# Kernel optimization log

Hardware: AMD Instinct MI355X
Metric: run time of the kernel (lower is better)

The kernel has to match this reference:

```python
import jax, jax.numpy as jnp
import numpy as np

T = 2048          # num tokens (single long prefill sequence)
HID = 2048        # hidden_size
NH = 16           # num query heads
NKV = 2           # num kv heads
HD = 128          # head_dim (kv_channels)
ROPE_BASE = 10000.0


def setup_inputs() -> dict:
    key = jax.random.key(0)
    k1, k2, k3, k4, k5 = jax.random.split(key, 5)
    s = 0.02
    return {
        "hidden_states": jax.random.normal(k1, (T, HID), dtype=jnp.float32),
        "positions": jnp.arange(T, dtype=jnp.int64 if jax.config.jax_enable_x64 else jnp.int32),
        "Wq": jax.random.normal(k2, (NH * HD, HID), dtype=jnp.float32) * s,
        "Wk": jax.random.normal(k3, (NKV * HD, HID), dtype=jnp.float32) * s,
        "Wv": jax.random.normal(k4, (NKV * HD, HID), dtype=jnp.float32) * s,
        "Wo": jax.random.normal(k5, (HID, NH * HD), dtype=jnp.float32) * s,
    }


def _rope_cos_sin(positions):
    # fp32 RoPE tables, HF-style (concat of freqs with itself)
    inv_freq = 1.0 / (ROPE_BASE ** (jnp.arange(0, HD, 2, dtype=jnp.float32) / HD))
    freqs = positions.astype(jnp.float32)[:, None] * inv_freq[None, :]   # [T, HD/2]
    emb = jnp.concatenate([freqs, freqs], axis=-1)                        # [T, HD]
    return jnp.cos(emb)[:, None, :], jnp.sin(emb)[:, None, :]             # [T,1,HD]


def _rotate_half(x):
    x1, x2 = jnp.split(x, 2, axis=-1)
    return jnp.concatenate([-x2, x1], axis=-1)


def reference(hidden_states, positions, Wq, Wk, Wv, Wo):
    dtype = hidden_states.dtype
    # fused QKV projection (weights concatenated once, single GEMM)
    W_fused = jnp.concatenate([Wq, Wk, Wv], axis=0)            # [q+2kv, HID]
    qkv = hidden_states @ W_fused.T                             # [T, q+2kv]
    q, k, v = jnp.split(qkv, [NH * HD, NH * HD + NKV * HD], axis=-1)

    # fp32 RoPE on q/k
    cos, sin = _rope_cos_sin(positions)                         # [T,1,HD]
    qf = q.reshape(T, NH, HD).astype(jnp.float32)
    kf = k.reshape(T, NKV, HD).astype(jnp.float32)
    qf = qf * cos + _rotate_half(qf) * sin
    kf = kf * cos + _rotate_half(kf) * sin
    q = qf.astype(dtype)                                        # [T,NH,HD]
    k = kf.astype(dtype)                                        # [T,NKV,HD]
    v = v.reshape(T, NKV, HD)

    # causal GQA attention (same math as the paged-attention kernel on one seq)
    group = NH // NKV
    k_rep = jnp.repeat(k, group, axis=1)                        # [T,NH,HD]
    v_rep = jnp.repeat(v, group, axis=1)                        # [T,NH,HD]
    scale = HD ** -0.5
    scores = jnp.einsum('qhd,khd->hqk', q, k_rep) * scale       # [NH,T,T]
    causal = jnp.tril(jnp.ones((T, T), dtype=bool))
    scores = jnp.where(causal[None], scores, jnp.finfo(scores.dtype).min)
    probs = jax.nn.softmax(scores, axis=-1)
    attn = jnp.einsum('hqk,khd->qhd', probs, v_rep).reshape(T, NH * HD)

    return attn @ Wo.T                                          # [T, HID]
```

## Files before the change

### kernel.cpp

```cpp
#include <hip/hip_runtime.h>

#define T_TOK 2048
#define HID   2048
#define NH    16
#define NKV   2
#define HD    128
#define QDIM  (NH * HD)
#define KVDIM (NKV * HD)
#define QKVDIM (QDIM + 2 * KVDIM)

typedef float          f32x4  __attribute__((ext_vector_type(4)));
typedef unsigned short u16x8  __attribute__((ext_vector_type(8)));
typedef __bf16         bf16x8 __attribute__((ext_vector_type(8)));

__device__ __forceinline__ unsigned short f2bf(float f) {
    unsigned int u = __builtin_bit_cast(unsigned int, f);
    u += 0x7fffu + ((u >> 16) & 1u);
    return (unsigned short)(u >> 16);
}

__device__ __forceinline__ f32x4 mfma16(u16x8 a, u16x8 b, f32x4 c) {
    return __builtin_amdgcn_mfma_f32_16x16x32_bf16(
        __builtin_bit_cast(bf16x8, a), __builtin_bit_cast(bf16x8, b), c, 0, 0, 0);
}

__global__ __launch_bounds__(256) void pack_bf16_all(
    const float* __restrict__ hidden, const float* __restrict__ Wq,
    const float* __restrict__ Wk, const float* __restrict__ Wv,
    const float* __restrict__ Wo,
    unsigned short* __restrict__ hb, unsigned short* __restrict__ Wf,
    unsigned short* __restrict__ Wob)
{
    const int b = blockIdx.x;
    const float* src; unsigned short* dst; size_t off;
    if      (b < 2048) { src = hidden; dst = hb;            off = (size_t)b * 2048; }
    else if (b < 4096) { src = Wq;     dst = Wf;            off = (size_t)(b - 2048) * 2048; }
    else if (b < 4352) { src = Wk;     dst = Wf + 4194304;  off = (size_t)(b - 4096) * 2048; }
    else if (b < 4608) { src = Wv;     dst = Wf + 4718592;  off = (size_t)(b - 4352) * 2048; }
    else               { src = Wo;     dst = Wob;           off = (size_t)(b - 4608) * 2048; }

    const size_t i = off + threadIdx.x * 8;
    float4 f0 = *reinterpret_cast<const float4*>(src + i);
    float4 f1 = *reinterpret_cast<const float4*>(src + i + 4);
    u16x8 o;
    o[0]=f2bf(f0.x); o[1]=f2bf(f0.y); o[2]=f2bf(f0.z); o[3]=f2bf(f0.w);
    o[4]=f2bf(f1.x); o[5]=f2bf(f1.y); o[6]=f2bf(f1.z); o[7]=f2bf(f1.w);
    *reinterpret_cast<u16x8*>(dst + i) = o;
}

__global__ __launch_bounds__(256) void gemm_bf16(
    const unsigned short* __restrict__ A,
    const unsigned short* __restrict__ B,
    float* __restrict__ C,
    int K, int NC)
{
    __shared__ alignas(16) unsigned short As[2][128 * 64];
    __shared__ alignas(16) unsigned short Bs[2][128 * 64];

    const int tid  = threadIdx.x;
    const int lane = tid & 63;
    const int w    = tid >> 6;
    const int lg   = lane >> 4, lc = lane & 15;
    const int m0   = blockIdx.y * 128, n0 = blockIdx.x * 128;

    const int rowL = lane >> 3;
    const int gS   = (lane & 7) ^ rowL;
    const int wr   = (w >> 1) * 64, wc = (w & 1) * 64;

    f32x4 acc[4][4] = {};

    auto stage = [&](int buf, int kb) {
        #pragma unroll
        for (int ci = 0; ci < 4; ci++) {
            const int chunk = w * 4 + ci;
            const int row   = chunk * 8 + rowL;
            const unsigned short* gpA = &A[(size_t)(m0 + row) * K + kb + gS * 8];
            __builtin_amdgcn_global_load_lds(
                (const __attribute__((address_space(1))) void*)gpA,
                (__attribute__((address_space(3))) void*)(&As[buf][chunk * 512]),
                16, 0, 0);
            const unsigned short* gpB = &B[(size_t)(n0 + row) * K + kb + gS * 8];
            __builtin_amdgcn_global_load_lds(
                (const __attribute__((address_space(1))) void*)gpB,
                (__attribute__((address_space(3))) void*)(&Bs[buf][chunk * 512]),
                16, 0, 0);
        }
    };

    stage(0, 0);
    const int nk = K >> 6;
    for (int t = 0; t < nk; ++t) {
        asm volatile("s_waitcnt vmcnt(0)" ::: "memory");
        __syncthreads();
        if (t + 1 < nk) stage((t + 1) & 1, (t + 1) * 64);

        const unsigned short* As_ = As[t & 1];
        const unsigned short* Bs_ = Bs[t & 1];
        #pragma unroll
        for (int kk = 0; kk < 2; kk++) {
            u16x8 af[4], bf[4];
            #pragma unroll
            for (int mi = 0; mi < 4; mi++) {
                const int r = wr + mi * 16 + lc;
                const int g = (kk * 4 + lg) ^ (lc & 7);
                af[mi] = *reinterpret_cast<const u16x8*>(&As_[r * 64 + g * 8]);
            }
            #pragma unroll
            for (int ni = 0; ni < 4; ni++) {
                const int r = wc + ni * 16 + lc;
                const int g = (kk * 4 + lg) ^ (lc & 7);
                bf[ni] = *reinterpret_cast<const u16x8*>(&Bs_[r * 64 + g * 8]);
            }
            #pragma unroll
            for (int mi = 0; mi < 4; mi++)
                #pragma unroll
                for (int ni = 0; ni < 4; ni++)
                    acc[mi][ni] = mfma16(af[mi], bf[ni], acc[mi][ni]);
        }
        __syncthreads();
    }

    #pragma unroll
    for (int mi = 0; mi < 4; mi++)
        #pragma unroll
        for (int ni = 0; ni < 4; ni++)
            #pragma unroll
            for (int j = 0; j < 4; j++)
                C[(size_t)(m0 + wr + mi * 16 + lg * 4 + j) * NC
                  + n0 + wc + ni * 16 + lc] = acc[mi][ni][j];
}

__global__ __launch_bounds__(256) void rope_kernel(
    const float* __restrict__ qkv,
    const int* __restrict__ positions,
    unsigned short* __restrict__ qr,
    unsigned short* __restrict__ kr)
{
    const int t   = blockIdx.x;
    const int tid = threadIdx.x;
    __shared__ float cosv[64], sinv[64];

    if (tid < 64) {
        float invf = expf(-(float)tid * 0.14391156831212787f);
        float f = (float)positions[t] * invf;
        cosv[tid] = cosf(f);
        sinv[tid] = sinf(f);
    }
    __syncthreads();

    const float* row = qkv + (size_t)t * QKVDIM;

    for (int i = tid; i < NH * 64; i += 256) {
        int hh = i >> 6, j = i & 63;
        float x1 = row[hh * HD + j];
        float x2 = row[hh * HD + j + 64];
        float c = cosv[j], s = sinv[j];
        qr[(size_t)t * QDIM + hh * HD + j]      = f2bf(x1 * c - x2 * s);
        qr[(size_t)t * QDIM + hh * HD + j + 64] = f2bf(x2 * c + x1 * s);
    }
    if (tid < NKV * 64) {
        int hh = tid >> 6, j = tid & 63;
        float x1 = row[QDIM + hh * HD + j];
        float x2 = row[QDIM + hh * HD + j + 64];
        float c = cosv[j], s = sinv[j];
        kr[(size_t)t * KVDIM + hh * HD + j]      = f2bf(x1 * c - x2 * s);
        kr[(size_t)t * KVDIM + hh * HD + j + 64] = f2bf(x2 * c + x1 * s);
    }
}

__global__ __launch_bounds__(256) void v_transpose(
    const float* __restrict__ qkv,
    unsigned short* __restrict__ vt)
{
    __shared__ unsigned short tile[64][72];
    const int tid = threadIdx.x;
    const int t0  = blockIdx.x * 64;
    const int d0  = blockIdx.y * 64;

    {
        int r = tid >> 2;
        int c = (tid & 3) * 16;
        const float* src = &qkv[(size_t)(t0 + r) * QKVDIM + QDIM + KVDIM + d0 + c];
        #pragma unroll
        for (int i = 0; i < 4; i++) {
            float4 f = *reinterpret_cast<const float4*>(src + i * 4);
            tile[r][c + i*4 + 0] = f2bf(f.x);
            tile[r][c + i*4 + 1] = f2bf(f.y);
            tile[r][c + i*4 + 2] = f2bf(f.z);
            tile[r][c + i*4 + 3] = f2bf(f.w);
        }
    }
    __syncthreads();
    {
        int dr = tid >> 3;
        int tc = (tid & 7) * 8;
        #pragma unroll
        for (int i = 0; i < 2; i++) {
            int d = dr + i * 32;
            u16x8 ov;
            #pragma unroll
            for (int e = 0; e < 8; e++) ov[e] = tile[tc + e][d];
            *reinterpret_cast<u16x8*>(&vt[(size_t)(d0 + d) * T_TOK + t0 + tc]) = ov;
        }
    }
}

__global__ __launch_bounds__(256) void attn_kernel(
    const unsigned short* __restrict__ q,
    const unsigned short* __restrict__ k,
    const unsigned short* __restrict__ vt,
    unsigned short* __restrict__ o,
    float* __restrict__ pO,
    float* __restrict__ pML)
{
    __shared__ alignas(16) unsigned short Ks[2][64 * 128];
    __shared__ alignas(16) unsigned short Vs[2][128 * 64];
    __shared__ alignas(16) unsigned short P[4][16][72];

    const int tid  = threadIdx.x;
    const int lane = tid & 63;
    const int w    = tid >> 6;
    const int lg   = lane >> 4, lc = lane & 15;
    const int b    = blockIdx.x;
    const int h    = b & 15;
    const int idx  = b >> 4;

    int tau, c0;
    if (idx <= 16)      { tau = 15 + idx; c0 = 0; }
    else if (idx == 17) { tau = 31;       c0 = 1; }
    else {
        int j = idx - 18, kk = 15 - (j >> 1);
        if ((j & 1) == 0) { tau = kk - 1;  c0 = 0; }
        else              { tau = kk + 15; c0 = 1; }
    }
    const int kstart = c0 << 4;
    const int kcnt   = min(16, tau + 1 - kstart);

    const int q0   = tau * 64 + w * 16;
    const int hk   = h >> 3;
    const float scale = 0.08838834764831845f;
    const int xr   = (lc & 7) << 4;

    const int krow_l = (lane >> 4);
    const int kgS    = (lane & 15);
    const int vrow_l = (lane >> 3);
    const int vgS    = (lane & 7);

    u16x8 qf[4];
    #pragma unroll
    for (int dc = 0; dc < 4; dc++)
        qf[dc] = *reinterpret_cast<const u16x8*>(
            &q[(size_t)(q0 + lc) * QDIM + h * HD + dc * 32 + lg * 8]);

    float mrow = -1e30f, ell = 0.f;
    f32x4 oacc[8] = {};

    auto stage = [&](int buf, int kb) {
        #pragma unroll
        for (int ci = 0; ci < 4; ci++) {
            const int chunk = w * 4 + ci;
            const int row   = chunk * 4 + krow_l;
            const int gSk   = kgS ^ (row & 7);
            const unsigned short* gp =
                &k[(size_t)(kb + row) * KVDIM + hk * HD + gSk * 8];
            __builtin_amdgcn_global_load_lds(
                (const __attribute__((address_space(1))) void*)gp,
                (__attribute__((address_space(3))) void*)(&Ks[buf][chunk * 512]),
                16, 0, 0);
        }
        #pragma unroll
        for (int ci = 0; ci < 4; ci++) {
            const int chunk = w * 4 + ci;
            const int dr    = chunk * 8 + vrow_l;
            const int gSv   = vgS ^ (dr & 7);
            const unsigned short* gp =
                &vt[(size_t)(hk * HD + dr) * T_TOK + kb + gSv * 8];
            __builtin_amdgcn_global_load_lds(
                (const __attribute__((address_space(1))) void*)gp,
                (__attribute__((address_space(3))) void*)(&Vs[buf][chunk * 512]),
                16, 0, 0);
        }
    };

    stage(0, kstart * 64);
    for (int it = 0; it < kcnt; ++it) {
        asm volatile("s_waitcnt vmcnt(0)" ::: "memory");
        __syncthreads();
        if (it + 1 < kcnt) stage((it + 1) & 1, (kstart + it + 1) * 64);

        const int kb = (kstart + it) * 64;
        const char* KsB = (const char*)Ks[it & 1];
        const char* VsB = (const char*)Vs[it & 1];

        float sc[4][4];
        #pragma unroll
        for (int c4 = 0; c4 < 4; c4++) {
            const int row = c4 * 16 + lc;
            f32x4 s = {0.f, 0.f, 0.f, 0.f};
            #pragma unroll
            for (int dc = 0; dc < 4; dc++) {
                u16x8 kf = *reinterpret_cast<const u16x8*>(
                    KsB + row * 256 + ((dc * 64 + lg * 16) ^ xr));
                s = mfma16(kf, qf[dc], s);
            }
            #pragma unroll
            for (int j = 0; j < 4; j++) {
                const int kpos = kb + c4 * 16 + lg * 4 + j;
                const int qrow = q0 + lc;
                sc[c4][j] = (kpos <= qrow) ? s[j] * scale : -1e30f;
            }
        }

        float t01 = fmaxf(fmaxf(sc[0][0], sc[0][1]), fmaxf(sc[0][2], sc[0][3]));
        float t23 = fmaxf(fmaxf(sc[1][0], sc[1][1]), fmaxf(sc[1][2], sc[1][3]));
        float t45 = fmaxf(fmaxf(sc[2][0], sc[2][1]), fmaxf(sc[2][2], sc[2][3]));
        float t67 = fmaxf(fmaxf(sc[3][0], sc[3][1]), fmaxf(sc[3][2], sc[3][3]));
        float tmx = fmaxf(fmaxf(t01, t23), fmaxf(t45, t67));
        tmx = fmaxf(tmx, __shfl_xor(tmx, 16));
        tmx = fmaxf(tmx, __shfl_xor(tmx, 32));

        float mn;
        if (__all(tmx <= mrow + 8.0f)) {
            mn = mrow;
        } else {
            mn = fmaxf(mrow, tmx);
            float alpha = __expf(mrow - mn);
            mrow = mn;
            ell *= alpha;
            float aj[4];
            #pragma unroll
            for (int j = 0; j < 4; j++)
                aj[j] = __shfl(alpha, lg * 4 + j);
            #pragma unroll
            for (int d8 = 0; d8 < 8; d8++)
                #pragma unroll
                for (int j = 0; j < 4; j++)
                    oacc[d8][j] *= aj[j];
        }

        float rs = 0.f;
        #pragma unroll
        for (int c4 = 0; c4 < 4; c4++) {
            float p0 = __expf(sc[c4][0] - mn);
            float p1 = __expf(sc[c4][1] - mn);
            float p2 = __expf(sc[c4][2] - mn);
            float p3 = __expf(sc[c4][3] - mn);
            rs += (p0 + p1) + (p2 + p3);
            ushort4 pk;
            pk.x = f2bf(p0); pk.y = f2bf(p1); pk.z = f2bf(p2); pk.w = f2bf(p3);
            *reinterpret_cast<ushort4*>(&P[w][lc][c4 * 16 + lg * 4]) = pk;
        }
        rs += __shfl_xor(rs, 16);
        rs += __shfl_xor(rs, 32);
        ell += rs;

        asm volatile("s_waitcnt lgkmcnt(0)" ::: "memory");
        __builtin_amdgcn_sched_barrier(0);

        u16x8 pf0 = *reinterpret_cast<const u16x8*>(&P[w][lc][lg * 8]);
        u16x8 pf1 = *reinterpret_cast<const u16x8*>(&P[w][lc][32 + lg * 8]);

        #pragma unroll
        for (int d8 = 0; d8 < 8; d8++) {
            const int drow = d8 * 16 + lc;
            u16x8 vf0 = *reinterpret_cast<const u16x8*>(
                VsB + drow * 128 + ((lg * 16) ^ xr));
            u16x8 vf1 = *reinterpret_cast<const u16x8*>(
                VsB + drow * 128 + ((lg * 16 + 64) ^ xr));
            oacc[d8] = mfma16(pf0, vf0, oacc[d8]);
            oacc[d8] = mfma16(pf1, vf1, oacc[d8]);
        }
        __syncthreads();
    }

    if (tau < 16) {
        float ej[4];
        #pragma unroll
        for (int j = 0; j < 4; j++)
            ej[j] = __shfl(ell, lg * 4 + j);
        #pragma unroll
        for (int d8 = 0; d8 < 8; d8++)
            #pragma unroll
            for (int j = 0; j < 4; j++) {
                float val = oacc[d8][j] / ej[j];
                o[(size_t)(q0 + lg * 4 + j) * QDIM + h * HD + d8 * 16 + lc] = f2bf(val);
            }
    } else {
        const int s = (h * 16 + (tau - 16)) * 2 + c0;
        float* po = pO + (size_t)s * 8192;
        #pragma unroll
        for (int d8 = 0; d8 < 8; d8++)
            #pragma unroll
            for (int j = 0; j < 4; j++)
                po[(w * 16 + lg * 4 + j) * 128 + d8 * 16 + lc] = oacc[d8][j];
        if (lg == 0) {
            pML[s * 128 + w * 16 + lc]      = mrow;
            pML[s * 128 + 64 + w * 16 + lc] = ell;
        }
    }
}

__global__ __launch_bounds__(256) void attn_combine(
    const float* __restrict__ pO,
    const float* __restrict__ pML,
    unsigned short* __restrict__ o)
{
    const int b  = blockIdx.x;
    const int h  = b >> 4, ti = b & 15;
    const int tau = 16 + ti;
    const int s0 = (h * 16 + ti) * 2, s1 = s0 + 1;

    const int tid = threadIdx.x;
    const int r   = tid >> 2;
    const int cg  = (tid & 3) * 32;

    const float m1 = pML[s0 * 128 + r],      m2 = pML[s1 * 128 + r];
    const float l1 = pML[s0 * 128 + 64 + r], l2 = pML[s1 * 128 + 64 + r];
    const float M  = fmaxf(m1, m2);
    const float w1 = __expf(m1 - M), w2 = __expf(m2 - M);
    const float rn = 1.0f / (w1 * l1 + w2 * l2);

    const float* o1 = pO + (size_t)s0 * 8192 + r * 128 + cg;
    const float* o2 = pO + (size_t)s1 * 8192 + r * 128 + cg;
    unsigned short* dst = o + (size_t)(tau * 64 + r) * QDIM + h * HD + cg;

    #pragma unroll
    for (int i = 0; i < 8; i++) {
        float4 a = *reinterpret_cast<const float4*>(o1 + i * 4);
        float4 c = *reinterpret_cast<const float4*>(o2 + i * 4);
        ushort4 pk;
        pk.x = f2bf((w1 * a.x + w2 * c.x) * rn);
        pk.y = f2bf((w1 * a.y + w2 * c.y) * rn);
        pk.z = f2bf((w1 * a.z + w2 * c.z) * rn);
        pk.w = f2bf((w1 * a.w + w2 * c.w) * rn);
        *reinterpret_cast<ushort4*>(dst + i * 4) = pk;
    }
}

extern "C" void kernel_launch(void* const* d_in, const int* in_sizes, int n_in,
                              void* d_out, int out_size, void* d_ws, size_t ws_size,
                              hipStream_t stream) {
    const float* hidden    = (const float*)d_in[0];
    const int*   positions = (const int*)d_in[1];
    const float* Wq        = (const float*)d_in[2];
    const float* Wk        = (const float*)d_in[3];
    const float* Wv        = (const float*)d_in[4];
    const float* Wo        = (const float*)d_in[5];
    float*       out       = (float*)d_out;

    char* ws = (char*)d_ws;
    float*          qkv = (float*)(ws);
    unsigned short* qr  = (unsigned short*)(ws + 20971520);
    unsigned short* kr  = (unsigned short*)(ws + 29360128);
    unsigned short* vt  = (unsigned short*)(ws + 30408704);
    unsigned short* att = (unsigned short*)(ws + 31457280);
    unsigned short* hb  = (unsigned short*)(ws + 39845888);
    unsigned short* Wf  = (unsigned short*)(ws + 48234496);
    unsigned short* Wob = (unsigned short*)(ws + 58720256);
    float* pO  = (float*)(ws);
    float* pML = (float*)(ws + 16777216);

    pack_bf16_all<<<6656, 256, 0, stream>>>(hidden, Wq, Wk, Wv, Wo, hb, Wf, Wob);
    gemm_bf16<<<dim3(QKVDIM / 128, T_TOK / 128), 256, 0, stream>>>(hb, Wf, qkv, HID, QKVDIM);
    rope_kernel<<<T_TOK, 256, 0, stream>>>(qkv, positions, qr, kr);
    v_transpose<<<dim3(T_TOK / 64, KVDIM / 64), 256, 0, stream>>>(qkv, vt);
    attn_kernel<<<NH * 48, 256, 0, stream>>>(qr, kr, vt, att, pO, pML);
    attn_combine<<<256, 256, 0, stream>>>(pO, pML, att);
    gemm_bf16<<<dim3(HID / 128, T_TOK / 128), 256, 0, stream>>>(att, Wob, out, QDIM, HID);
}
```

Baseline: 147.8 us.

## Emit bf16 QKV, prefetch before wait, fold softmax scale into Q, use exp2

The QKV GEMM now writes bf16 instead of fp32, which halves that intermediate traffic and lets rope and the V transpose read bf16. In both GEMMs and attention, the next tile's load is issued before waiting on only the older loads, so the copy overlaps compute. The GEMM also remaps block indices in an XCD-aware pattern across the 8 dies. The softmax scale times log2(e) is folded into Q during rope, so attention uses raw exp2 and masks only diagonal tiles. The lazy-rescale threshold is widened to match the base-2 scale, and storing QKV in bf16 adds a rounding step before rope.

```diff
diff --git a/kernel.cpp b/kernel.cpp
--- a/kernel.cpp
+++ b/kernel.cpp
@@ -14,15 +14,20 @@
 typedef __bf16         bf16x8 __attribute__((ext_vector_type(8)));
 
 __device__ __forceinline__ unsigned short f2bf(float f) {
-    unsigned int u = __builtin_bit_cast(unsigned int, f);
-    u += 0x7fffu + ((u >> 16) & 1u);
-    return (unsigned short)(u >> 16);
+    __bf16 h = (__bf16)f;
+    return __builtin_bit_cast(unsigned short, h);
+}
+__device__ __forceinline__ float bf2f(unsigned short u) {
+    return (float)__builtin_bit_cast(__bf16, u);
 }
 
 __device__ __forceinline__ f32x4 mfma16(u16x8 a, u16x8 b, f32x4 c) {
     return __builtin_amdgcn_mfma_f32_16x16x32_bf16(
         __builtin_bit_cast(bf16x8, a), __builtin_bit_cast(bf16x8, b), c, 0, 0, 0);
 }
+
+#define QSCL 0.12751743f
+#define DEFER_THR 11.5416f
 
 __global__ __launch_bounds__(256) void pack_bf16_all(
     const float* __restrict__ hidden, const float* __restrict__ Wq,
@@ -48,11 +53,12 @@
     *reinterpret_cast<u16x8*>(dst + i) = o;
 }
 
+template<bool BF16OUT>
 __global__ __launch_bounds__(256) void gemm_bf16(
     const unsigned short* __restrict__ A,
     const unsigned short* __restrict__ B,
-    float* __restrict__ C,
-    int K, int NC)
+    void* __restrict__ Cv,
+    int K, int NC, int nbx)
 {
     __shared__ alignas(16) unsigned short As[2][128 * 64];
     __shared__ alignas(16) unsigned short Bs[2][128 * 64];
@@ -61,7 +67,10 @@
     const int lane = tid & 63;
     const int w    = tid >> 6;
     const int lg   = lane >> 4, lc = lane & 15;
-    const int m0   = blockIdx.y * 128, n0 = blockIdx.x * 128;
+
+    const int cpx = gridDim.x >> 3;
+    const int wg  = (blockIdx.x & 7) * cpx + (blockIdx.x >> 3);
+    const int m0  = (wg / nbx) * 128, n0 = (wg % nbx) * 128;
 
     const int rowL = lane >> 3;
     const int gS   = (lane & 7) ^ rowL;
@@ -90,9 +99,13 @@
     stage(0, 0);
     const int nk = K >> 6;
     for (int t = 0; t < nk; ++t) {
-        asm volatile("s_waitcnt vmcnt(0)" ::: "memory");
+        if (t + 1 < nk) {
+            stage((t + 1) & 1, (t + 1) * 64);
+            asm volatile("s_waitcnt vmcnt(8)" ::: "memory");
+        } else {
+            asm volatile("s_waitcnt vmcnt(0)" ::: "memory");
+        }
         __syncthreads();
-        if (t + 1 < nk) stage((t + 1) & 1, (t + 1) * 64);
 
         const unsigned short* As_ = As[t & 1];
         const unsigned short* Bs_ = Bs[t & 1];
@@ -125,13 +138,18 @@
         #pragma unroll
         for (int ni = 0; ni < 4; ni++)
             #pragma unroll
-            for (int j = 0; j < 4; j++)
-                C[(size_t)(m0 + wr + mi * 16 + lg * 4 + j) * NC
-                  + n0 + wc + ni * 16 + lc] = acc[mi][ni][j];
+            for (int j = 0; j < 4; j++) {
+                const size_t idx = (size_t)(m0 + wr + mi * 16 + lg * 4 + j) * NC
+                                   + n0 + wc + ni * 16 + lc;
+                if constexpr (BF16OUT)
+                    ((unsigned short*)Cv)[idx] = f2bf(acc[mi][ni][j]);
+                else
+                    ((float*)Cv)[idx] = acc[mi][ni][j];
+            }
 }
 
 __global__ __launch_bounds__(256) void rope_kernel(
-    const float* __restrict__ qkv,
+    const unsigned short* __restrict__ qkvb,
     const int* __restrict__ positions,
     unsigned short* __restrict__ qr,
     unsigned short* __restrict__ kr)
@@ -148,20 +166,20 @@
     }
     __syncthreads();
 
-    const float* row = qkv + (size_t)t * QKVDIM;
+    const unsigned short* row = qkvb + (size_t)t * QKVDIM;
 
     for (int i = tid; i < NH * 64; i += 256) {
         int hh = i >> 6, j = i & 63;
-        float x1 = row[hh * HD + j];
-        float x2 = row[hh * HD + j + 64];
+        float x1 = bf2f(row[hh * HD + j]);
+        float x2 = bf2f(row[hh * HD + j + 64]);
         float c = cosv[j], s = sinv[j];
-        qr[(size_t)t * QDIM + hh * HD + j]      = f2bf(x1 * c - x2 * s);
-        qr[(size_t)t * QDIM + hh * HD + j + 64] = f2bf(x2 * c + x1 * s);
+        qr[(size_t)t * QDIM + hh * HD + j]      = f2bf((x1 * c - x2 * s) * QSCL);
+        qr[(size_t)t * QDIM + hh * HD + j + 64] = f2bf((x2 * c + x1 * s) * QSCL);
     }
     if (tid < NKV * 64) {
         int hh = tid >> 6, j = tid & 63;
-        float x1 = row[QDIM + hh * HD + j];
-        float x2 = row[QDIM + hh * HD + j + 64];
+        float x1 = bf2f(row[QDIM + hh * HD + j]);
+        float x2 = bf2f(row[QDIM + hh * HD + j + 64]);
         float c = cosv[j], s = sinv[j];
         kr[(size_t)t * KVDIM + hh * HD + j]      = f2bf(x1 * c - x2 * s);
         kr[(size_t)t * KVDIM + hh * HD + j + 64] = f2bf(x2 * c + x1 * s);
@@ -169,7 +187,7 @@
 }
 
 __global__ __launch_bounds__(256) void v_transpose(
-    const float* __restrict__ qkv,
+    const unsigned short* __restrict__ qkvb,
     unsigned short* __restrict__ vt)
 {
     __shared__ unsigned short tile[64][72];
@@ -180,15 +198,10 @@
     {
         int r = tid >> 2;
         int c = (tid & 3) * 16;
-        const float* src = &qkv[(size_t)(t0 + r) * QKVDIM + QDIM + KVDIM + d0 + c];
-        #pragma unroll
-        for (int i = 0; i < 4; i++) {
-            float4 f = *reinterpret_cast<const float4*>(src + i * 4);
-            tile[r][c + i*4 + 0] = f2bf(f.x);
-            tile[r][c + i*4 + 1] = f2bf(f.y);
-            tile[r][c + i*4 + 2] = f2bf(f.z);
-            tile[r][c + i*4 + 3] = f2bf(f.w);
-        }
+        const unsigned short* src =
+            &qkvb[(size_t)(t0 + r) * QKVDIM + QDIM + KVDIM + d0 + c];
+        *reinterpret_cast<u16x8*>(&tile[r][c])     = *reinterpret_cast<const u16x8*>(src);
+        *reinterpret_cast<u16x8*>(&tile[r][c + 8]) = *reinterpret_cast<const u16x8*>(src + 8);
     }
     __syncthreads();
     {
@@ -238,7 +251,6 @@
 
     const int q0   = tau * 64 + w * 16;
     const int hk   = h >> 3;
-    const float scale = 0.08838834764831845f;
     const int xr   = (lc & 7) << 4;
 
     const int krow_l = (lane >> 4);
@@ -284,15 +296,20 @@
 
     stage(0, kstart * 64);
     for (int it = 0; it < kcnt; ++it) {
-        asm volatile("s_waitcnt vmcnt(0)" ::: "memory");
+        if (it + 1 < kcnt) {
+            stage((it + 1) & 1, (kstart + it + 1) * 64);
+            asm volatile("s_waitcnt vmcnt(8)" ::: "memory");
+        } else {
+            asm volatile("s_waitcnt vmcnt(0)" ::: "memory");
+        }
         __syncthreads();
-        if (it + 1 < kcnt) stage((it + 1) & 1, (kstart + it + 1) * 64);
 
         const int kb = (kstart + it) * 64;
         const char* KsB = (const char*)Ks[it & 1];
         const char* VsB = (const char*)Vs[it & 1];
 
         float sc[4][4];
+        const bool dia = (kb + 63 > q0);
         #pragma unroll
         for (int c4 = 0; c4 < 4; c4++) {
             const int row = c4 * 16 + lc;
@@ -303,11 +320,15 @@
                     KsB + row * 256 + ((dc * 64 + lg * 16) ^ xr));
                 s = mfma16(kf, qf[dc], s);
             }
-            #pragma unroll
-            for (int j = 0; j < 4; j++) {
-                const int kpos = kb + c4 * 16 + lg * 4 + j;
-                const int qrow = q0 + lc;
-                sc[c4][j] = (kpos <= qrow) ? s[j] * scale : -1e30f;
+            if (dia) {
+                #pragma unroll
+                for (int j = 0; j < 4; j++) {
+                    const int kpos = kb + c4 * 16 + lg * 4 + j;
+                    sc[c4][j] = (kpos <= q0 + lc) ? s[j] : -1e30f;
+                }
+            } else {
+                #pragma unroll
+                for (int j = 0; j < 4; j++) sc[c4][j] = s[j];
             }
         }
 
@@ -320,11 +341,11 @@
         tmx = fmaxf(tmx, __shfl_xor(tmx, 32));
 
         float mn;
-        if (__all(tmx <= mrow + 8.0f)) {
+        if (__all(tmx <= mrow + DEFER_THR)) {
             mn = mrow;
         } else {
             mn = fmaxf(mrow, tmx);
-            float alpha = __expf(mrow - mn);
+            float alpha = __builtin_amdgcn_exp2f(mrow - mn);
             mrow = mn;
             ell *= alpha;
             float aj[4];
@@ -341,10 +362,10 @@
         float rs = 0.f;
         #pragma unroll
         for (int c4 = 0; c4 < 4; c4++) {
-            float p0 = __expf(sc[c4][0] - mn);
-            float p1 = __expf(sc[c4][1] - mn);
-            float p2 = __expf(sc[c4][2] - mn);
-            float p3 = __expf(sc[c4][3] - mn);
+            float p0 = __builtin_amdgcn_exp2f(sc[c4][0] - mn);
+            float p1 = __builtin_amdgcn_exp2f(sc[c4][1] - mn);
+            float p2 = __builtin_amdgcn_exp2f(sc[c4][2] - mn);
+            float p3 = __builtin_amdgcn_exp2f(sc[c4][3] - mn);
             rs += (p0 + p1) + (p2 + p3);
             ushort4 pk;
             pk.x = f2bf(p0); pk.y = f2bf(p1); pk.z = f2bf(p2); pk.w = f2bf(p3);
@@ -417,7 +438,8 @@
     const float m1 = pML[s0 * 128 + r],      m2 = pML[s1 * 128 + r];
     const float l1 = pML[s0 * 128 + 64 + r], l2 = pML[s1 * 128 + 64 + r];
     const float M  = fmaxf(m1, m2);
-    const float w1 = __expf(m1 - M), w2 = __expf(m2 - M);
+    const float w1 = __builtin_amdgcn_exp2f(m1 - M);
+    const float w2 = __builtin_amdgcn_exp2f(m2 - M);
     const float rn = 1.0f / (w1 * l1 + w2 * l2);
 
     const float* o1 = pO + (size_t)s0 * 8192 + r * 128 + cg;
@@ -449,7 +471,7 @@
     float*       out       = (float*)d_out;
 
     char* ws = (char*)d_ws;
-    float*          qkv = (float*)(ws);
+    unsigned short* qkvb = (unsigned short*)(ws);
     unsigned short* qr  = (unsigned short*)(ws + 20971520);
     unsigned short* kr  = (unsigned short*)(ws + 29360128);
     unsigned short* vt  = (unsigned short*)(ws + 30408704);
@@ -461,10 +483,10 @@
     float* pML = (float*)(ws + 16777216);
 
     pack_bf16_all<<<6656, 256, 0, stream>>>(hidden, Wq, Wk, Wv, Wo, hb, Wf, Wob);
-    gemm_bf16<<<dim3(QKVDIM / 128, T_TOK / 128), 256, 0, stream>>>(hb, Wf, qkv, HID, QKVDIM);
-    rope_kernel<<<T_TOK, 256, 0, stream>>>(qkv, positions, qr, kr);
-    v_transpose<<<dim3(T_TOK / 64, KVDIM / 64), 256, 0, stream>>>(qkv, vt);
+    gemm_bf16<true><<<320, 256, 0, stream>>>(hb, Wf, qkvb, HID, QKVDIM, QKVDIM / 128);
+    rope_kernel<<<T_TOK, 256, 0, stream>>>(qkvb, positions, qr, kr);
+    v_transpose<<<dim3(T_TOK / 64, KVDIM / 64), 256, 0, stream>>>(qkvb, vt);
     attn_kernel<<<NH * 48, 256, 0, stream>>>(qr, kr, vt, att, pO, pML);
     attn_combine<<<256, 256, 0, stream>>>(pO, pML, att);
-    gemm_bf16<<<dim3(HID / 128, T_TOK / 128), 256, 0, stream>>>(att, Wob, out, QDIM, HID);
-}
+    gemm_bf16<false><<<256, 256, 0, stream>>>(att, Wob, out, QDIM, HID, HID / 128);
+}
```

After: 145.6 us. About the same (-1.5%).
